# Optimization experiments

Measured on AMD Instinct MI355X. Metric: run time of the kernel, lower is better.

## Reference

```python
import jax, jax.numpy as jnp
import numpy as np

NUM_BITS_ACTS = 8
NUM_BITS_PARAMS = 8
NUM_BITS_ACCUM = 32


def quantized_range(num_bits):
    # distiller-style signed range: [-2^(n-1), 2^(n-1)-1]
    n = 2.0 ** num_bits
    return -n / 2.0, n / 2.0 - 1.0


def sym_scale(num_bits, sat_abs):
    # scale = (2^(n-1)-1) / max_abs
    return (2.0 ** (num_bits - 1) - 1.0) / sat_abs


def quant_clamp(t, scale, qmin, qmax):
    return jnp.clip(jnp.round(t * scale), qmin, qmax)


def setup_inputs() -> dict:
    key = jax.random.key(0)
    kx, kw = jax.random.split(key)
    x = jax.random.normal(kx, (8192, 4096), dtype=jnp.float32)
    W = jax.random.normal(kw, (4096, 4096), dtype=jnp.float32)  # [out, in]
    return {"x": x, "W": W}


def reference(x, W):
    acts_min, acts_max = quantized_range(NUM_BITS_ACTS)
    params_min, params_max = quantized_range(NUM_BITS_PARAMS)
    accum_min, accum_max = quantized_range(NUM_BITS_ACCUM)

    # __init__: quantize weights once (symmetric, max-abs)
    w_scale = sym_scale(NUM_BITS_PARAMS, jnp.max(jnp.abs(W)))
    W_q = quant_clamp(W, w_scale, params_min, params_max)

    # pre_quantized_forward: input scale from max-abs, quantize-clamp input
    in_scale = sym_scale(NUM_BITS_ACTS, jnp.max(jnp.abs(x)))
    x_q = quant_clamp(x, in_scale, acts_min, acts_max)

    # wrapped Linear in integer domain, clamp to accumulator range
    accum = jnp.clip(x_q @ W_q.T, accum_min, accum_max)  # [8192, 4096]

    # post_quantized_forward: requantize accumulator to output range
    accum_scale = in_scale * w_scale
    accum_max_abs = jnp.max(jnp.abs(accum))
    y_f_max_abs = accum_max_abs / accum_scale
    out_scale = sym_scale(NUM_BITS_ACTS, y_f_max_abs)
    requant_scale = out_scale / accum_scale

    out_q = quant_clamp(accum, requant_scale, acts_min, acts_max)
    out_f = out_q / out_scale  # dequantize
    return out_f
```

## Files before the change

### kernel.cpp

```cpp
#include <hip/hip_runtime.h>
#include <stdint.h>


using i32x4 = __attribute__((ext_vector_type(4))) int;

#define M_DIM 8192
#define N_DIM 4096
#define K_DIM 4096

#define BM 256
#define BN 256
#define BKB 128
#define NKT (K_DIM / BKB)

__global__ void k_init(unsigned* sc) {
    sc[0] = 0u;
    sc[1] = 0u;
    sc[2] = 0u;
}

__global__ __launch_bounds__(256) void k_absmax(const float4* __restrict__ src, int n4,
                                                unsigned* __restrict__ out) {
    unsigned m = 0;
    int stride = gridDim.x * blockDim.x;
    for (int i = blockIdx.x * blockDim.x + threadIdx.x; i < n4; i += stride) {
        float4 v = src[i];
        unsigned a = __float_as_uint(v.x) & 0x7fffffffu;
        unsigned b = __float_as_uint(v.y) & 0x7fffffffu;
        unsigned c = __float_as_uint(v.z) & 0x7fffffffu;
        unsigned d = __float_as_uint(v.w) & 0x7fffffffu;
        m = max(m, max(max(a, b), max(c, d)));
    }
    for (int off = 32; off; off >>= 1)
        m = max(m, (unsigned)__shfl_xor((int)m, off));
    __shared__ unsigned wm[4];
    int ln = threadIdx.x & 63, wv = threadIdx.x >> 6;
    if (ln == 0) wm[wv] = m;
    __syncthreads();
    if (threadIdx.x == 0)
        atomicMax(out, max(max(wm[0], wm[1]), max(wm[2], wm[3])));
}

__global__ __launch_bounds__(256) void k_quant(const float4* __restrict__ src,
                                               unsigned* __restrict__ dst, int n4,
                                               const unsigned* __restrict__ maxbits) {
    float scale = 127.0f / __uint_as_float(*maxbits);
    int stride = gridDim.x * blockDim.x;
    for (int i = blockIdx.x * blockDim.x + threadIdx.x; i < n4; i += stride) {
        float4 v = src[i];
        int q0 = min(127, max(-128, (int)rintf(v.x * scale)));
        int q1 = min(127, max(-128, (int)rintf(v.y * scale)));
        int q2 = min(127, max(-128, (int)rintf(v.z * scale)));
        int q3 = min(127, max(-128, (int)rintf(v.w * scale)));
        dst[i] = (unsigned)(q0 & 0xff) | ((unsigned)(q1 & 0xff) << 8) |
                 ((unsigned)(q2 & 0xff) << 16) | ((unsigned)(q3 & 0xff) << 24);
    }
}

__global__ __launch_bounds__(512, 2) void k_gemm(const char* __restrict__ Aq,
                                                 const char* __restrict__ Bq,
                                                 int* __restrict__ C,
                                                 unsigned* __restrict__ maxAcc) {
    __shared__ __align__(16) char lds[131072];
    __shared__ int wmax[8];
    char* lA = lds;
    char* lB = lds + 65536;

    const int t = threadIdx.x;
    const int ln = t & 63;
    const int wv = t >> 6;
    const int wr = wv >> 2;
    const int wc = wv & 3;
    const int lr = ln & 15;
    const int lk = ln >> 4;

    const int bid = blockIdx.x;
    const int swz = (bid & 7) * 64 + (bid >> 3);
    const int bx = swz & 15;
    const int by = swz >> 4;
    const size_t arow0 = (size_t)by * BM;
    const size_t brow0 = (size_t)bx * BN;

    i32x4 acc[8][4];
#pragma unroll
    for (int i = 0; i < 8; ++i)
#pragma unroll
        for (int j = 0; j < 4; ++j) acc[i][j] = (i32x4)(0);

    auto STAGE = [&](int kt, int j) {
        const int slot = kt & 1;
        const char* gbase = (j < 2) ? Aq : Bq;
        char* lbase = ((j < 2) ? lA : lB) + slot * 32768 + (j & 1) * 16384;
        const size_t grow0 = ((j < 2) ? arow0 : brow0) + (size_t)((j & 1) << 7);
        const int k0 = kt * BKB;
#pragma unroll
        for (int it = 0; it < 2; ++it) {
            const int chunkBase = it * 512 + (wv << 6);
            const int chunk = chunkBase + ln;
            const int row = chunk >> 3;
            const int gc = (chunk & 7) ^ (row & 7);
            const char* g = gbase + ((grow0 + (size_t)row) << 12) + k0 + (gc << 4);
            __builtin_amdgcn_global_load_lds(
                (const __attribute__((address_space(1))) void*)g,
                (__attribute__((address_space(3))) void*)(lbase + chunkBase * 16), 16, 0, 0);
        }
    };

#pragma unroll
    for (int h = 0; h < 8; ++h) STAGE(h >> 2, h & 3);
    asm volatile("s_waitcnt vmcnt(8)" ::: "memory");
    __builtin_amdgcn_s_barrier();
    __builtin_amdgcn_sched_barrier(0);

    for (int kt = 0; kt < NKT; ++kt) {
        const int slot = kt & 1;
        const char* sA = lA + slot * 32768;
        const char* sB = lB + slot * 32768;
        i32x4 a0[4][2], a4[4][2], b0[2][2], b2[2][2];

#pragma unroll
        for (int mi = 0; mi < 4; ++mi)
#pragma unroll
            for (int kh = 0; kh < 2; ++kh) {
                const int r = (wr << 7) + (mi << 4) + lr;
                const int cs = ((kh << 2) | lk) ^ (r & 7);
                a0[mi][kh] = *(const i32x4*)(sA + r * 128 + (cs << 4));
            }
#pragma unroll
        for (int ni = 0; ni < 2; ++ni)
#pragma unroll
            for (int kh = 0; kh < 2; ++kh) {
                const int r = (wc << 6) + (ni << 4) + lr;
                const int cs = ((kh << 2) | lk) ^ (r & 7);
                b0[ni][kh] = *(const i32x4*)(sB + r * 128 + (cs << 4));
            }
        __builtin_amdgcn_s_barrier();
        __builtin_amdgcn_sched_barrier(0);
        asm volatile("s_waitcnt lgkmcnt(0)" ::: "memory");
        __builtin_amdgcn_sched_barrier(0);
        __builtin_amdgcn_s_setprio(1);
#pragma unroll
        for (int mi = 0; mi < 4; ++mi)
#pragma unroll
            for (int ni = 0; ni < 2; ++ni)
#pragma unroll
                for (int kh = 0; kh < 2; ++kh)
                    acc[mi][ni] = __builtin_amdgcn_mfma_i32_16x16x64_i8(
                        a0[mi][kh], b0[ni][kh], acc[mi][ni], 0, 0, 0);
        __builtin_amdgcn_s_setprio(0);
        __builtin_amdgcn_s_barrier();
        __builtin_amdgcn_sched_barrier(0);

#pragma unroll
        for (int ni = 0; ni < 2; ++ni)
#pragma unroll
            for (int kh = 0; kh < 2; ++kh) {
                const int r = (wc << 6) + ((ni + 2) << 4) + lr;
                const int cs = ((kh << 2) | lk) ^ (r & 7);
                b2[ni][kh] = *(const i32x4*)(sB + r * 128 + (cs << 4));
            }
        __builtin_amdgcn_s_barrier();
        __builtin_amdgcn_sched_barrier(0);
        asm volatile("s_waitcnt lgkmcnt(0)" ::: "memory");
        __builtin_amdgcn_sched_barrier(0);
        __builtin_amdgcn_s_setprio(1);
#pragma unroll
        for (int mi = 0; mi < 4; ++mi)
#pragma unroll
            for (int ni = 0; ni < 2; ++ni)
#pragma unroll
                for (int kh = 0; kh < 2; ++kh)
                    acc[mi][ni + 2] = __builtin_amdgcn_mfma_i32_16x16x64_i8(
                        a0[mi][kh], b2[ni][kh], acc[mi][ni + 2], 0, 0, 0);
        __builtin_amdgcn_s_setprio(0);
        __builtin_amdgcn_s_barrier();
        __builtin_amdgcn_sched_barrier(0);

#pragma unroll
        for (int mi = 0; mi < 4; ++mi)
#pragma unroll
            for (int kh = 0; kh < 2; ++kh) {
                const int r = (wr << 7) + ((mi + 4) << 4) + lr;
                const int cs = ((kh << 2) | lk) ^ (r & 7);
                a4[mi][kh] = *(const i32x4*)(sA + r * 128 + (cs << 4));
            }
        if (kt + 2 < NKT) { STAGE(kt + 2, 2); STAGE(kt + 2, 3); }
        __builtin_amdgcn_s_barrier();
        __builtin_amdgcn_sched_barrier(0);
        asm volatile("s_waitcnt lgkmcnt(0)" ::: "memory");
        __builtin_amdgcn_sched_barrier(0);
        __builtin_amdgcn_s_setprio(1);
#pragma unroll
        for (int mi = 0; mi < 4; ++mi)
#pragma unroll
            for (int ni = 0; ni < 2; ++ni)
#pragma unroll
                for (int kh = 0; kh < 2; ++kh)
                    acc[mi + 4][ni] = __builtin_amdgcn_mfma_i32_16x16x64_i8(
                        a4[mi][kh], b0[ni][kh], acc[mi + 4][ni], 0, 0, 0);
        __builtin_amdgcn_s_setprio(0);
        __builtin_amdgcn_s_barrier();
        __builtin_amdgcn_sched_barrier(0);

        if (kt + 2 < NKT) { STAGE(kt + 2, 0); STAGE(kt + 2, 1); }
        asm volatile("s_waitcnt vmcnt(8)" ::: "memory");
        __builtin_amdgcn_s_barrier();
        __builtin_amdgcn_sched_barrier(0);
        __builtin_amdgcn_s_setprio(1);
#pragma unroll
        for (int mi = 0; mi < 4; ++mi)
#pragma unroll
            for (int ni = 0; ni < 2; ++ni)
#pragma unroll
                for (int kh = 0; kh < 2; ++kh)
                    acc[mi + 4][ni + 2] = __builtin_amdgcn_mfma_i32_16x16x64_i8(
                        a4[mi][kh], b2[ni][kh], acc[mi + 4][ni + 2], 0, 0, 0);
        __builtin_amdgcn_s_setprio(0);
        __builtin_amdgcn_s_barrier();
        __builtin_amdgcn_sched_barrier(0);
    }

    int amax = 0;
#pragma unroll
    for (int mi = 0; mi < 8; ++mi) {
#pragma unroll
        for (int ni = 0; ni < 4; ++ni) {
            const int row0 = (int)arow0 + (wr << 7) + (mi << 4) + (lk << 2);
            const int col  = (int)brow0 + (wc << 6) + (ni << 4) + lr;
            i32x4 v = acc[mi][ni];
#pragma unroll
            for (int j = 0; j < 4; ++j) {
                C[(size_t)(row0 + j) * N_DIM + col] = v[j];
                int a = v[j] < 0 ? -v[j] : v[j];
                amax = max(amax, a);
            }
        }
    }
    for (int off = 32; off; off >>= 1)
        amax = max(amax, __shfl_xor(amax, off));
    if (ln == 0) wmax[wv] = amax;
    __syncthreads();
    if (t == 0) {
        int m = wmax[0];
#pragma unroll
        for (int i = 1; i < 8; ++i) m = max(m, wmax[i]);
        atomicMax(maxAcc, (unsigned)m);
    }
}

__global__ __launch_bounds__(256) void k_requant(int4* __restrict__ buf, int n4,
                                                 const unsigned* __restrict__ sc) {
    const float maxX = __uint_as_float(sc[0]);
    const float maxW = __uint_as_float(sc[1]);
    const float maxA = (float)(int)sc[2];
    const float in_scale = 127.0f / maxX;
    const float w_scale  = 127.0f / maxW;
    const float accum_scale = in_scale * w_scale;
    const float requant = 127.0f / maxA;
    const float out_scale = requant * accum_scale;
    int stride = gridDim.x * blockDim.x;
    for (int i = blockIdx.x * blockDim.x + threadIdx.x; i < n4; i += stride) {
        int4 v = buf[i];
        float4 o;
        o.x = fminf(127.f, fmaxf(-128.f, rintf((float)v.x * requant))) / out_scale;
        o.y = fminf(127.f, fmaxf(-128.f, rintf((float)v.y * requant))) / out_scale;
        o.z = fminf(127.f, fmaxf(-128.f, rintf((float)v.z * requant))) / out_scale;
        o.w = fminf(127.f, fmaxf(-128.f, rintf((float)v.w * requant))) / out_scale;
        ((float4*)buf)[i] = o;
    }
}

extern "C" void kernel_launch(void* const* d_in, const int* in_sizes, int n_in,
                              void* d_out, int out_size, void* d_ws, size_t ws_size,
                              hipStream_t stream) {
    const float* x = (const float*)d_in[0];
    const float* W = (const float*)d_in[1];

    unsigned* sc = (unsigned*)d_ws;
    char* xq = (char*)d_ws + 256;
    char* wq = xq + (size_t)M_DIM * K_DIM;

    k_init<<<1, 1, 0, stream>>>(sc);
    k_absmax<<<2048, 256, 0, stream>>>((const float4*)x, M_DIM * K_DIM / 4, sc + 0);
    k_absmax<<<1024, 256, 0, stream>>>((const float4*)W, N_DIM * K_DIM / 4, sc + 1);
    k_quant<<<2048, 256, 0, stream>>>((const float4*)x, (unsigned*)xq, M_DIM * K_DIM / 4, sc + 0);
    k_quant<<<1024, 256, 0, stream>>>((const float4*)W, (unsigned*)wq, N_DIM * K_DIM / 4, sc + 1);

    k_gemm<<<(M_DIM / BM) * (N_DIM / BN), 512, 0, stream>>>(xq, wq, (int*)d_out, sc + 2);

    k_requant<<<2048, 256, 0, stream>>>((int4*)d_out, M_DIM * N_DIM / 4, sc);
}
```

Measured before the change: 308.6 us.

## Merge x/W absmax and quant launches, precompute GEMM address offsets

Fuses the separate absmax and quantize launches for x and W into single 3072-block kernels that pick their source by block index, removing two launches and the tail gaps between them. In the GEMM, global and LDS address offsets are precomputed once as 32-bit ints, which cuts per-iteration address arithmetic and 64-bit math. The MFMA loop order is changed to kh-outer, and the final iterations now drain with vmcnt(0). The 32-bit offsets assume the operand sizes fit in unsigned range.

Result: faster. 297.4 us (-3.6%).

```diff
diff --git a/kernel.cpp b/kernel.cpp
--- a/kernel.cpp
+++ b/kernel.cpp
@@ -19,11 +19,16 @@
     sc[2] = 0u;
 }
 
-__global__ __launch_bounds__(256) void k_absmax(const float4* __restrict__ src, int n4,
-                                                unsigned* __restrict__ out) {
+__global__ __launch_bounds__(256) void k_absmax2(const float4* __restrict__ x,
+                                                 const float4* __restrict__ w,
+                                                 unsigned* __restrict__ sc) {
+    const bool isX = blockIdx.x < 2048;
+    const float4* src = isX ? x : w;
+    const int n4 = isX ? (M_DIM * K_DIM / 4) : (N_DIM * K_DIM / 4);
+    const int brel = isX ? blockIdx.x : (blockIdx.x - 2048);
+    const int nb = isX ? 2048 : 1024;
     unsigned m = 0;
-    int stride = gridDim.x * blockDim.x;
-    for (int i = blockIdx.x * blockDim.x + threadIdx.x; i < n4; i += stride) {
+    for (int i = brel * 256 + threadIdx.x; i < n4; i += nb * 256) {
         float4 v = src[i];
         unsigned a = __float_as_uint(v.x) & 0x7fffffffu;
         unsigned b = __float_as_uint(v.y) & 0x7fffffffu;
@@ -38,15 +43,22 @@
     if (ln == 0) wm[wv] = m;
     __syncthreads();
     if (threadIdx.x == 0)
-        atomicMax(out, max(max(wm[0], wm[1]), max(wm[2], wm[3])));
-}
-
-__global__ __launch_bounds__(256) void k_quant(const float4* __restrict__ src,
-                                               unsigned* __restrict__ dst, int n4,
-                                               const unsigned* __restrict__ maxbits) {
-    float scale = 127.0f / __uint_as_float(*maxbits);
-    int stride = gridDim.x * blockDim.x;
-    for (int i = blockIdx.x * blockDim.x + threadIdx.x; i < n4; i += stride) {
+        atomicMax(sc + (isX ? 0 : 1), max(max(wm[0], wm[1]), max(wm[2], wm[3])));
+}
+
+__global__ __launch_bounds__(256) void k_quant2(const float4* __restrict__ x,
+                                                const float4* __restrict__ w,
+                                                unsigned* __restrict__ xq,
+                                                unsigned* __restrict__ wq,
+                                                const unsigned* __restrict__ sc) {
+    const bool isX = blockIdx.x < 2048;
+    const float4* src = isX ? x : w;
+    unsigned* dst = isX ? xq : wq;
+    const int n4 = isX ? (M_DIM * K_DIM / 4) : (N_DIM * K_DIM / 4);
+    const int brel = isX ? blockIdx.x : (blockIdx.x - 2048);
+    const int nb = isX ? 2048 : 1024;
+    const float scale = 127.0f / __uint_as_float(sc[isX ? 0 : 1]);
+    for (int i = brel * 256 + threadIdx.x; i < n4; i += nb * 256) {
         float4 v = src[i];
         int q0 = min(127, max(-128, (int)rintf(v.x * scale)));
         int q1 = min(127, max(-128, (int)rintf(v.y * scale)));
@@ -63,8 +75,6 @@
                                                  unsigned* __restrict__ maxAcc) {
     __shared__ __align__(16) char lds[131072];
     __shared__ int wmax[8];
-    char* lA = lds;
-    char* lB = lds + 65536;
 
     const int t = threadIdx.x;
     const int ln = t & 63;
@@ -78,8 +88,24 @@
     const int swz = (bid & 7) * 64 + (bid >> 3);
     const int bx = swz & 15;
     const int by = swz >> 4;
-    const size_t arow0 = (size_t)by * BM;
-    const size_t brow0 = (size_t)bx * BN;
+    const int arow0 = by * BM;
+    const int brow0 = bx * BN;
+
+    const int cs0 = lk ^ (lr & 7);
+    const int aoff0 = (((wr << 7) + lr) << 7) + (cs0 << 4);
+    const int aoff1 = aoff0 ^ 64;
+    const int boff0 = (((wc << 6) + lr) << 7) + (cs0 << 4);
+    const int boff1 = boff0 ^ 64;
+
+    int voffA[2], voffB[2];
+#pragma unroll
+    for (int it = 0; it < 2; ++it) {
+        const int chunk = it * 512 + (wv << 6) + ln;
+        const int row = chunk >> 3;
+        const int gc = (chunk & 7) ^ (row & 7);
+        voffA[it] = (arow0 + row) * 4096 + (gc << 4);
+        voffB[it] = (brow0 + row) * 4096 + (gc << 4);
+    }
 
     i32x4 acc[8][4];
 #pragma unroll
@@ -89,20 +115,17 @@
 
     auto STAGE = [&](int kt, int j) {
         const int slot = kt & 1;
-        const char* gbase = (j < 2) ? Aq : Bq;
-        char* lbase = ((j < 2) ? lA : lB) + slot * 32768 + (j & 1) * 16384;
-        const size_t grow0 = ((j < 2) ? arow0 : brow0) + (size_t)((j & 1) << 7);
-        const int k0 = kt * BKB;
+        const int koff = kt * 128 + (j & 1) * 524288;
+        const bool isA = (j < 2);
+        const char* gbase = isA ? Aq : Bq;
+        const int* voff = isA ? voffA : voffB;
+        char* lbase = lds + (isA ? 0 : 65536) + (slot << 15) + ((j & 1) << 14) + (wv << 10);
 #pragma unroll
         for (int it = 0; it < 2; ++it) {
-            const int chunkBase = it * 512 + (wv << 6);
-            const int chunk = chunkBase + ln;
-            const int row = chunk >> 3;
-            const int gc = (chunk & 7) ^ (row & 7);
-            const char* g = gbase + ((grow0 + (size_t)row) << 12) + k0 + (gc << 4);
+            const char* g = gbase + (unsigned)(voff[it] + koff);
             __builtin_amdgcn_global_load_lds(
                 (const __attribute__((address_space(1))) void*)g,
-                (__attribute__((address_space(3))) void*)(lbase + chunkBase * 16), 16, 0, 0);
+                (__attribute__((address_space(3))) void*)(lbase + (it << 13)), 16, 0, 0);
         }
     };
 
@@ -113,38 +136,34 @@
     __builtin_amdgcn_sched_barrier(0);
 
     for (int kt = 0; kt < NKT; ++kt) {
-        const int slot = kt & 1;
-        const char* sA = lA + slot * 32768;
-        const char* sB = lB + slot * 32768;
+        const int sl = (kt & 1) << 15;
+        const char* pA0 = lds + sl + aoff0;
+        const char* pA1 = lds + sl + aoff1;
+        const char* pB0 = lds + 65536 + sl + boff0;
+        const char* pB1 = lds + 65536 + sl + boff1;
         i32x4 a0[4][2], a4[4][2], b0[2][2], b2[2][2];
 
 #pragma unroll
-        for (int mi = 0; mi < 4; ++mi)
-#pragma unroll
-            for (int kh = 0; kh < 2; ++kh) {
-                const int r = (wr << 7) + (mi << 4) + lr;
-                const int cs = ((kh << 2) | lk) ^ (r & 7);
-                a0[mi][kh] = *(const i32x4*)(sA + r * 128 + (cs << 4));
-            }
-#pragma unroll
-        for (int ni = 0; ni < 2; ++ni)
-#pragma unroll
-            for (int kh = 0; kh < 2; ++kh) {
-                const int r = (wc << 6) + (ni << 4) + lr;
-                const int cs = ((kh << 2) | lk) ^ (r & 7);
-                b0[ni][kh] = *(const i32x4*)(sB + r * 128 + (cs << 4));
-            }
+        for (int mi = 0; mi < 4; ++mi) {
+            a0[mi][0] = *(const i32x4*)(pA0 + (mi << 11));
+            a0[mi][1] = *(const i32x4*)(pA1 + (mi << 11));
+        }
+#pragma unroll
+        for (int ni = 0; ni < 2; ++ni) {
+            b0[ni][0] = *(const i32x4*)(pB0 + (ni << 11));
+            b0[ni][1] = *(const i32x4*)(pB1 + (ni << 11));
+        }
         __builtin_amdgcn_s_barrier();
         __builtin_amdgcn_sched_barrier(0);
         asm volatile("s_waitcnt lgkmcnt(0)" ::: "memory");
         __builtin_amdgcn_sched_barrier(0);
         __builtin_amdgcn_s_setprio(1);
 #pragma unroll
-        for (int mi = 0; mi < 4; ++mi)
-#pragma unroll
-            for (int ni = 0; ni < 2; ++ni)
-#pragma unroll
-                for (int kh = 0; kh < 2; ++kh)
+        for (int kh = 0; kh < 2; ++kh)
+#pragma unroll
+            for (int mi = 0; mi < 4; ++mi)
+#pragma unroll
+                for (int ni = 0; ni < 2; ++ni)
                     acc[mi][ni] = __builtin_amdgcn_mfma_i32_16x16x64_i8(
                         a0[mi][kh], b0[ni][kh], acc[mi][ni], 0, 0, 0);
         __builtin_amdgcn_s_setprio(0);
@@ -152,24 +171,21 @@
         __builtin_amdgcn_sched_barrier(0);
 
 #pragma unroll
-        for (int ni = 0; ni < 2; ++ni)
-#pragma unroll
-            for (int kh = 0; kh < 2; ++kh) {
-                const int r = (wc << 6) + ((ni + 2) << 4) + lr;
-                const int cs = ((kh << 2) | lk) ^ (r & 7);
-                b2[ni][kh] = *(const i32x4*)(sB + r * 128 + (cs << 4));
-            }
+        for (int ni = 0; ni < 2; ++ni) {
+            b2[ni][0] = *(const i32x4*)(pB0 + ((ni + 2) << 11));
+            b2[ni][1] = *(const i32x4*)(pB1 + ((ni + 2) << 11));
+        }
         __builtin_amdgcn_s_barrier();
         __builtin_amdgcn_sched_barrier(0);
         asm volatile("s_waitcnt lgkmcnt(0)" ::: "memory");
         __builtin_amdgcn_sched_barrier(0);
         __builtin_amdgcn_s_setprio(1);
 #pragma unroll
-        for (int mi = 0; mi < 4; ++mi)
-#pragma unroll
-            for (int ni = 0; ni < 2; ++ni)
-#pragma unroll
-                for (int kh = 0; kh < 2; ++kh)
+        for (int kh = 0; kh < 2; ++kh)
+#pragma unroll
+            for (int mi = 0; mi < 4; ++mi)
+#pragma unroll
+                for (int ni = 0; ni < 2; ++ni)
                     acc[mi][ni + 2] = __builtin_amdgcn_mfma_i32_16x16x64_i8(
                         a0[mi][kh], b2[ni][kh], acc[mi][ni + 2], 0, 0, 0);
         __builtin_amdgcn_s_setprio(0);
@@ -177,13 +193,10 @@
         __builtin_amdgcn_sched_barrier(0);
 
 #pragma unroll
-        for (int mi = 0; mi < 4; ++mi)
-#pragma unroll
-            for (int kh = 0; kh < 2; ++kh) {
-                const int r = (wr << 7) + ((mi + 4) << 4) + lr;
-                const int cs = ((kh << 2) | lk) ^ (r & 7);
-                a4[mi][kh] = *(const i32x4*)(sA + r * 128 + (cs << 4));
-            }
+        for (int mi = 0; mi < 4; ++mi) {
+            a4[mi][0] = *(const i32x4*)(pA0 + ((mi + 4) << 11));
+            a4[mi][1] = *(const i32x4*)(pA1 + ((mi + 4) << 11));
+        }
         if (kt + 2 < NKT) { STAGE(kt + 2, 2); STAGE(kt + 2, 3); }
         __builtin_amdgcn_s_barrier();
         __builtin_amdgcn_sched_barrier(0);
@@ -191,28 +204,32 @@
         __builtin_amdgcn_sched_barrier(0);
         __builtin_amdgcn_s_setprio(1);
 #pragma unroll
-        for (int mi = 0; mi < 4; ++mi)
-#pragma unroll
-            for (int ni = 0; ni < 2; ++ni)
-#pragma unroll
-                for (int kh = 0; kh < 2; ++kh)
+        for (int kh = 0; kh < 2; ++kh)
+#pragma unroll
+            for (int mi = 0; mi < 4; ++mi)
+#pragma unroll
+                for (int ni = 0; ni < 2; ++ni)
                     acc[mi + 4][ni] = __builtin_amdgcn_mfma_i32_16x16x64_i8(
                         a4[mi][kh], b0[ni][kh], acc[mi + 4][ni], 0, 0, 0);
         __builtin_amdgcn_s_setprio(0);
         __builtin_amdgcn_s_barrier();
         __builtin_amdgcn_sched_barrier(0);
 
-        if (kt + 2 < NKT) { STAGE(kt + 2, 0); STAGE(kt + 2, 1); }
-        asm volatile("s_waitcnt vmcnt(8)" ::: "memory");
+        if (kt + 2 < NKT) {
+            STAGE(kt + 2, 0); STAGE(kt + 2, 1);
+            asm volatile("s_waitcnt vmcnt(8)" ::: "memory");
+        } else {
+            asm volatile("s_waitcnt vmcnt(0)" ::: "memory");
+        }
         __builtin_amdgcn_s_barrier();
         __builtin_amdgcn_sched_barrier(0);
         __builtin_amdgcn_s_setprio(1);
 #pragma unroll
-        for (int mi = 0; mi < 4; ++mi)
-#pragma unroll
-            for (int ni = 0; ni < 2; ++ni)
-#pragma unroll
-                for (int kh = 0; kh < 2; ++kh)
+        for (int kh = 0; kh < 2; ++kh)
+#pragma unroll
+            for (int mi = 0; mi < 4; ++mi)
+#pragma unroll
+                for (int ni = 0; ni < 2; ++ni)
                     acc[mi + 4][ni + 2] = __builtin_amdgcn_mfma_i32_16x16x64_i8(
                         a4[mi][kh], b2[ni][kh], acc[mi + 4][ni + 2], 0, 0, 0);
         __builtin_amdgcn_s_setprio(0);
@@ -225,8 +242,8 @@
     for (int mi = 0; mi < 8; ++mi) {
 #pragma unroll
         for (int ni = 0; ni < 4; ++ni) {
-            const int row0 = (int)arow0 + (wr << 7) + (mi << 4) + (lk << 2);
-            const int col  = (int)brow0 + (wc << 6) + (ni << 4) + lr;
+            const int row0 = arow0 + (wr << 7) + (mi << 4) + (lk << 2);
+            const int col  = brow0 + (wc << 6) + (ni << 4) + lr;
             i32x4 v = acc[mi][ni];
 #pragma unroll
             for (int j = 0; j < 4; ++j) {
@@ -281,12 +298,9 @@
     char* wq = xq + (size_t)M_DIM * K_DIM;
 
     k_init<<<1, 1, 0, stream>>>(sc);
-    k_absmax<<<2048, 256, 0, stream>>>((const float4*)x, M_DIM * K_DIM / 4, sc + 0);
-    k_absmax<<<1024, 256, 0, stream>>>((const float4*)W, N_DIM * K_DIM / 4, sc + 1);
-    k_quant<<<2048, 256, 0, stream>>>((const float4*)x, (unsigned*)xq, M_DIM * K_DIM / 4, sc + 0);
-    k_quant<<<1024, 256, 0, stream>>>((const float4*)W, (unsigned*)wq, N_DIM * K_DIM / 4, sc + 1);
-
+    k_absmax2<<<3072, 256, 0, stream>>>((const float4*)x, (const float4*)W, sc);
+    k_quant2<<<3072, 256, 0, stream>>>((const float4*)x, (const float4*)W,
+                                       (unsigned*)xq, (unsigned*)wq, sc);
     k_gemm<<<(M_DIM / BM) * (N_DIM / BN), 512, 0, stream>>>(xq, wq, (int*)d_out, sc + 2);
-
     k_requant<<<2048, 256, 0, stream>>>((int4*)d_out, M_DIM * N_DIM / 4, sc);
 }
```
